# Kernel optimization log

Measured on AMD Instinct MI355X. Metric: run time of the kernel, lower is better.

The kernel has to match this reference:

```python
import jax, jax.numpy as jnp
import numpy as np
import math

EPS = 1e-7
K_NEIGHBORS = 32  # matches init kwarg k

def _project(x, c):
    norm = jnp.linalg.norm(x, axis=-1, keepdims=True).clip(EPS)
    sqrt_c = jnp.sqrt(c).clip(EPS)
    max_norm = (1.0 - EPS) / sqrt_c
    return x * jnp.minimum(max_norm / norm, 1.0)

def _mobius_add(x, y, c):
    x2 = jnp.sum(x * x, axis=-1, keepdims=True)
    y2 = jnp.sum(y * y, axis=-1, keepdims=True)
    xy = jnp.sum(x * y, axis=-1, keepdims=True)
    num = (1 + 2 * c * xy + c * y2) * x + (1 - c * x2) * y
    den = 1 + 2 * c * xy + c * c * x2 * y2
    return _project(num / den.clip(EPS), c)

def _dist(x, y, c):
    sqrt_c = jnp.sqrt(c).clip(EPS)
    diff = _mobius_add(x, -y, c)
    dn = jnp.linalg.norm(diff, axis=-1)
    arg = jnp.minimum(sqrt_c * dn.clip(EPS, 1 - EPS), 1.0 - EPS)
    return 2.0 * jnp.arctanh(arg) / sqrt_c

def _logmap0(y, c):
    sqrt_c = jnp.sqrt(c).clip(EPS)
    yn = jnp.linalg.norm(y, axis=-1, keepdims=True)
    is_zero = yn < EPS
    syn = yn.clip(EPS)
    arg = jnp.minimum(sqrt_c * syn, 1.0 - EPS)
    mag = jnp.arctanh(arg) / sqrt_c
    return jnp.where(is_zero, jnp.zeros_like(y), mag * y / syn)

def _layernorm(x, g, b):
    m = x.mean(-1, keepdims=True)
    v = x.var(-1, keepdims=True)
    return (x - m) / jnp.sqrt(v + 1e-6) * g + b

def setup_inputs() -> dict:
    key = jax.random.key(0)
    B, N, D, P, H = 2, 2048, 512, 3, 8
    ks = jax.random.split(key, 16)
    s = 0.02
    d = {}
    d['x'] = jax.random.normal(ks[0], (B, N, D), dtype=jnp.float32)
    d['positions'] = jax.random.normal(ks[1], (B, N, P), dtype=jnp.float32) * 0.1
    d['c'] = jnp.float32(1.0)
    d['Wq'] = jax.random.normal(ks[2], (D, D), jnp.float32) * s; d['bq'] = jnp.zeros((D,), jnp.float32)
    d['Wk'] = jax.random.normal(ks[3], (D, D), jnp.float32) * s; d['bk'] = jnp.zeros((D,), jnp.float32)
    d['Wv'] = jax.random.normal(ks[4], (D, D), jnp.float32) * s; d['bv'] = jnp.zeros((D,), jnp.float32)
    d['Wg'] = jax.random.normal(ks[5], (P, D), jnp.float32) * s; d['bg'] = jnp.zeros((D,), jnp.float32)
    d['Wo'] = jax.random.normal(ks[6], (D, D), jnp.float32) * s; d['bo'] = jnp.zeros((D,), jnp.float32)
    d['Wf1'] = jax.random.normal(ks[7], (D, 4 * D), jnp.float32) * s; d['bf1'] = jnp.zeros((4 * D,), jnp.float32)
    d['Wf2'] = jax.random.normal(ks[8], (4 * D, D), jnp.float32) * s; d['bf2'] = jnp.zeros((D,), jnp.float32)
    d['g1'] = jnp.ones((D,), jnp.float32); d['b1'] = jnp.zeros((D,), jnp.float32)
    d['g2'] = jnp.ones((D,), jnp.float32); d['b2'] = jnp.zeros((D,), jnp.float32)
    d['ascale'] = jnp.ones((H,), jnp.float32)
    d['fscale'] = jnp.ones((H,), jnp.float32)
    return d

def reference(x, positions, c, Wq, bq, Wk, bk, Wv, bv, Wg, bg, Wo, bo, Wf1, bf1, Wf2, bf2, g1, b1, g2, b2, ascale, fscale):
    B, N, D = x.shape
    H = ascale.shape[0]
    hd = D // H
    K = K_NEIGHBORS

    xn = _layernorm(x, g1, b1)
    q = (xn @ Wq + bq).reshape(B, N, H, hd)
    k = (xn @ Wk + bk).reshape(B, N, H, hd)
    v = (xn @ Wv + bv).reshape(B, N, H, hd)

    # full pairwise hyperbolic distance matrix [B, N, N]
    dmat = _dist(positions[:, :, None, :], positions[:, None, :, :], c)
    idx = jax.lax.top_k(-dmat, K)[1]  # [B, N, K]

    bidx = jnp.arange(B)[:, None, None]
    key_pos = positions[bidx, idx]                 # [B, N, K, P]
    qpos = positions[:, :, None, :]                # [B, N, 1, P]
    geo = _logmap0(_mobius_add(-qpos, key_pos, c), c)
    geo_v = (geo @ Wg + bg).reshape(B, N, K, H, hd)

    kg = k[bidx, idx]                              # [B, N, K, H, hd]
    vg = v[bidx, idx]

    align = jnp.einsum('bnhd,bnkhd->bhnk', q, geo_v)
    feat = jnp.einsum('bnhd,bnkhd->bhnk', q, kg) / math.sqrt(hd)
    scores = fscale[None, :, None, None] * feat + ascale[None, :, None, None] * align
    w = jax.nn.softmax(scores.astype(jnp.float32), axis=-1)
    attn = jnp.einsum('bhnk,bnkhd->bnhd', w, vg).reshape(B, N, D)

    x1 = x + attn @ Wo + bo
    h = _layernorm(x1, g2, b2)
    x2 = x1 + jax.nn.gelu(h @ Wf1 + bf1) @ Wf2 + bf2
    return x2
```

## Files before the change

kernel.cpp:

```cpp
#include <hip/hip_runtime.h>
#include <math.h>

#define EPSF 1e-7f

constexpr int Bb = 2, Nn = 2048, Dd = 512, Hh = 8, HD = 64, KK = 32;
constexpr int ROWS = Bb * Nn;

typedef __attribute__((ext_vector_type(8))) short bf16x8;
typedef __attribute__((ext_vector_type(4))) float f32x4;
typedef __attribute__((ext_vector_type(8))) unsigned short u16x8;
typedef unsigned long long u64;

__device__ inline unsigned short f2bf(float f) {
    union { float f; unsigned int u; } v; v.f = f;
    unsigned int u = v.u;
    unsigned int r = (u + 0x7fffu + ((u >> 16) & 1u)) >> 16;
    return (unsigned short)r;
}

__device__ inline float bf2f(short s) {
    union { unsigned int u; float f; } x;
    x.u = ((unsigned int)(unsigned short)s) << 16;
    return x.f;
}

__device__ inline float gelu_tanh(float v) {
    float u = v + 0.044715f * v * v * v;
    return 0.5f * v * (1.f + tanhf(0.79788456080286535588f * u));
}

__device__ __forceinline__ void tcvt(float (*tile)[65], const float* __restrict__ in,
                                     unsigned short* __restrict__ out,
                                     int K, int N, int bx, int by) {
    int k0 = by * 64, n0 = bx * 64;
    int t = threadIdx.x;
    int lr = t >> 6, lc = t & 63;
#pragma unroll 4
    for (int p = 0; p < 16; ++p) {
        int r = p * 4 + lr;
        tile[r][lc] = in[(size_t)(k0 + r) * N + n0 + lc];
    }
    __syncthreads();
#pragma unroll 4
    for (int p = 0; p < 16; ++p) {
        int n = p * 4 + lr;
        out[(size_t)(n0 + n) * K + k0 + lc] = f2bf(tile[lc][n]);
    }
}

__device__ __forceinline__ void ln_row(const float* __restrict__ x,
                                       const float* __restrict__ g,
                                       const float* __restrict__ b,
                                       unsigned short* __restrict__ out,
                                       int row, int lane) {
    const float* xr = x + (size_t)row * Dd;
    float4 v0 = *(const float4*)(xr + lane * 8);
    float4 v1 = *(const float4*)(xr + lane * 8 + 4);
    float s = v0.x + v0.y + v0.z + v0.w + v1.x + v1.y + v1.z + v1.w;
    float s2 = v0.x * v0.x + v0.y * v0.y + v0.z * v0.z + v0.w * v0.w +
               v1.x * v1.x + v1.y * v1.y + v1.z * v1.z + v1.w * v1.w;
    for (int o = 32; o; o >>= 1) { s += __shfl_xor(s, o); s2 += __shfl_xor(s2, o); }
    float mean = s * (1.f / Dd);
    float var = s2 * (1.f / Dd) - mean * mean;
    float rstd = rsqrtf(var + 1e-6f);
    float4 g0 = *(const float4*)(g + lane * 8);
    float4 g1v = *(const float4*)(g + lane * 8 + 4);
    float4 b0 = *(const float4*)(b + lane * 8);
    float4 b1v = *(const float4*)(b + lane * 8 + 4);
    u16x8 o;
    o[0] = f2bf((v0.x - mean) * rstd * g0.x + b0.x);
    o[1] = f2bf((v0.y - mean) * rstd * g0.y + b0.y);
    o[2] = f2bf((v0.z - mean) * rstd * g0.z + b0.z);
    o[3] = f2bf((v0.w - mean) * rstd * g0.w + b0.w);
    o[4] = f2bf((v1.x - mean) * rstd * g1v.x + b1v.x);
    o[5] = f2bf((v1.y - mean) * rstd * g1v.y + b1v.y);
    o[6] = f2bf((v1.z - mean) * rstd * g1v.z + b1v.z);
    o[7] = f2bf((v1.w - mean) * rstd * g1v.w + b1v.w);
    *(u16x8*)(out + (size_t)row * Dd + lane * 8) = o;
}

__global__ __launch_bounds__(256) void ln_kernel(const float* __restrict__ x,
                                                 const float* __restrict__ g,
                                                 const float* __restrict__ b,
                                                 unsigned short* __restrict__ out) {
    ln_row(x, g, b, out, blockIdx.x * 4 + (threadIdx.x >> 6), threadIdx.x & 63);
}

__global__ __launch_bounds__(256) void prep_kernel(
    const float* __restrict__ Wq, const float* __restrict__ Wk,
    const float* __restrict__ Wv, const float* __restrict__ Wo,
    const float* __restrict__ Wf1, const float* __restrict__ Wf2,
    const float* __restrict__ bq, const float* __restrict__ bk, const float* __restrict__ bv,
    const float* __restrict__ x, const float* __restrict__ g1, const float* __restrict__ b1,
    unsigned short* __restrict__ wqkv_t, unsigned short* __restrict__ wo_t,
    unsigned short* __restrict__ wf1_t, unsigned short* __restrict__ wf2_t,
    float* __restrict__ bqkv, unsigned short* __restrict__ xn) {
    __shared__ float tile[64][65];
    int bid = blockIdx.x;
    if (bid < 256) {
        int z = bid >> 6, r = bid & 63;
        const float* in = (z == 0) ? Wq : (z == 1) ? Wk : (z == 2) ? Wv : Wo;
        unsigned short* out = (z == 0) ? wqkv_t : (z == 1) ? wqkv_t + 262144
                            : (z == 2) ? wqkv_t + 524288 : wo_t;
        tcvt(tile, in, out, 512, 512, r & 7, r >> 3);
    } else if (bid < 512) {
        int r = bid - 256;
        tcvt(tile, Wf1, wf1_t, 512, 2048, r & 31, r >> 5);
    } else if (bid < 768) {
        int r = bid - 512;
        tcvt(tile, Wf2, wf2_t, 2048, 512, r & 7, r >> 3);
    } else if (bid < 774) {
        int t = (bid - 768) * 256 + threadIdx.x;
        if (t < 512) bqkv[t] = bq[t];
        else if (t < 1024) bqkv[t] = bk[t - 512];
        else if (t < 1536) bqkv[t] = bv[t - 1024];
    } else {
        ln_row(x, g1, b1, xn, (bid - 774) * 4 + (threadIdx.x >> 6), threadIdx.x & 63);
    }
}

template <int EPI, int OBF16>
__device__ __forceinline__ void gemm64_body(short* __restrict__ As, short* __restrict__ Bs,
                                            const unsigned short* __restrict__ A,
                                            const unsigned short* __restrict__ Bt,
                                            const float* __restrict__ bias,
                                            const float* __restrict__ resid,
                                            void* __restrict__ C,
                                            int N, int K, int gridX, int nwg, int wgid) {
    int cpx = nwg >> 3;
    int nid = (wgid & 7) * cpx + (wgid >> 3);
    int bx = nid % gridX, by = nid / gridX;
    int bm = by * 64, bn = bx * 64;
    int tid = threadIdx.x;
    int wave = tid >> 6, lane = tid & 63;
    int wr = wave >> 1, wc = wave & 1;
    f32x4 acc[2][2] = {};

    int srow = wave * 8 + (lane >> 3);
    int scol = ((lane & 7) ^ (lane >> 3)) * 8;
    const unsigned short* gA0 = A + (size_t)(bm + srow) * K + scol;
    const unsigned short* gA1 = A + (size_t)(bm + srow + 32) * K + scol;
    const unsigned short* gB0 = Bt + (size_t)(bn + srow) * K + scol;
    const unsigned short* gB1 = Bt + (size_t)(bn + srow + 32) * K + scol;

#define STAGE(buf, kof)                                                                                 \
    do {                                                                                                \
        __builtin_amdgcn_global_load_lds((const __attribute__((address_space(1))) void*)(gA0 + (kof)), \
            (__attribute__((address_space(3))) void*)(As + (buf) * 4096 + wave * 512), 16, 0, 0);       \
        __builtin_amdgcn_global_load_lds((const __attribute__((address_space(1))) void*)(gA1 + (kof)), \
            (__attribute__((address_space(3))) void*)(As + (buf) * 4096 + 2048 + wave * 512), 16, 0, 0);\
        __builtin_amdgcn_global_load_lds((const __attribute__((address_space(1))) void*)(gB0 + (kof)), \
            (__attribute__((address_space(3))) void*)(Bs + (buf) * 4096 + wave * 512), 16, 0, 0);       \
        __builtin_amdgcn_global_load_lds((const __attribute__((address_space(1))) void*)(gB1 + (kof)), \
            (__attribute__((address_space(3))) void*)(Bs + (buf) * 4096 + 2048 + wave * 512), 16, 0, 0);\
    } while (0)

    int nt = K >> 6;
    int cur = 0;
    STAGE(0, 0);
    __syncthreads();
    for (int t = 0; t < nt; ++t) {
        if (t + 1 < nt) STAGE(cur ^ 1, (t + 1) * 64);
        const short* as = As + cur * 4096;
        const short* bs = Bs + cur * 4096;
#pragma unroll
        for (int kk = 0; kk < 64; kk += 32) {
            int kx = (kk + (lane >> 4) * 8) ^ ((lane & 7) << 3);
            bf16x8 a0 = *(const bf16x8*)(as + (wr * 32 + (lane & 15)) * 64 + kx);
            bf16x8 a1 = *(const bf16x8*)(as + (wr * 32 + 16 + (lane & 15)) * 64 + kx);
            bf16x8 b0 = *(const bf16x8*)(bs + (wc * 32 + (lane & 15)) * 64 + kx);
            bf16x8 b1 = *(const bf16x8*)(bs + (wc * 32 + 16 + (lane & 15)) * 64 + kx);
            acc[0][0] = __builtin_amdgcn_mfma_f32_16x16x32_bf16(a0, b0, acc[0][0], 0, 0, 0);
            acc[0][1] = __builtin_amdgcn_mfma_f32_16x16x32_bf16(a0, b1, acc[0][1], 0, 0, 0);
            acc[1][0] = __builtin_amdgcn_mfma_f32_16x16x32_bf16(a1, b0, acc[1][0], 0, 0, 0);
            acc[1][1] = __builtin_amdgcn_mfma_f32_16x16x32_bf16(a1, b1, acc[1][1], 0, 0, 0);
        }
        __syncthreads();
        cur ^= 1;
    }
#undef STAGE

    int cbase = bn + wc * 32 + (lane & 15);
    int rbase = bm + wr * 32 + (lane >> 4) * 4;
    float bias_v[2] = {bias[cbase], bias[cbase + 16]};
#pragma unroll
    for (int mi = 0; mi < 2; ++mi) {
#pragma unroll
        for (int r = 0; r < 4; ++r) {
            int row = rbase + mi * 16 + r;
#pragma unroll
            for (int ni = 0; ni < 2; ++ni) {
                int col = cbase + ni * 16;
                float v = acc[mi][ni][r] + bias_v[ni];
                if (EPI == 1) v += resid[(size_t)row * N + col];
                if (EPI == 2) v = gelu_tanh(v);
                if (OBF16) ((unsigned short*)C)[(size_t)row * N + col] = f2bf(v);
                else ((float*)C)[(size_t)row * N + col] = v;
            }
        }
    }
}

template <int EPI, int OBF16>
__global__ __launch_bounds__(256) void gemm64(const unsigned short* __restrict__ A,
                                              const unsigned short* __restrict__ Bt,
                                              const float* __restrict__ bias,
                                              const float* __restrict__ resid,
                                              void* __restrict__ C,
                                              int N, int K, int gridX) {
    __shared__ short As[2 * 64 * 64];
    __shared__ short Bs[2 * 64 * 64];
    gemm64_body<EPI, OBF16>(As, Bs, A, Bt, bias, resid, C, N, K, gridX, gridDim.x, blockIdx.x);
}

template <int CTRL>
__device__ inline u64 dpp_u64(u64 v) {
    int lo = (int)(unsigned int)v;
    int hi = (int)(unsigned int)(v >> 32);
    lo = __builtin_amdgcn_update_dpp(lo, lo, CTRL, 0xF, 0xF, false);
    hi = __builtin_amdgcn_update_dpp(hi, hi, CTRL, 0xF, 0xF, false);
    return ((u64)(unsigned int)hi << 32) | (unsigned int)lo;
}

__device__ inline u64 wave_min_u64(u64 v) {
    u64 o;
    o = dpp_u64<0xB1>(v);  if (o < v) v = o;
    o = dpp_u64<0x4E>(v);  if (o < v) v = o;
    o = dpp_u64<0x141>(v); if (o < v) v = o;
    o = dpp_u64<0x140>(v); if (o < v) v = o;
    o = __shfl_xor(v, 16); if (o < v) v = o;
    o = __shfl_xor(v, 32); if (o < v) v = o;
    return v;
}

__device__ __forceinline__ void topk_body(char* smem, const float* __restrict__ pos,
                                          const float* __restrict__ cp,
                                          int* __restrict__ idx_out, int bid) {
    float* s_px = (float*)smem;
    float* s_py = s_px + Nn;
    float* s_pz = s_py + Nn;
    float* s_u  = s_pz + Nn;
    int* s_out  = (int*)(s_u + Nn);
    int b = bid >> 9;
    int q0 = (bid & 511) * 4;
    int t = threadIdx.x;
    float c = *cp;
    const float* pb = pos + (size_t)b * Nn * 3;
    for (int j = t; j < Nn; j += 256) {
        float px = pb[j * 3 + 0], py = pb[j * 3 + 1], pz = pb[j * 3 + 2];
        s_px[j] = px; s_py[j] = py; s_pz[j] = pz;
        s_u[j] = c * (px * px + py * py + pz * pz);
    }
    __syncthreads();
    int wave = t >> 6, lane = t & 63;
    int n = q0 + wave;
    float qx = s_px[n], qy = s_py[n], qz = s_pz[n];
    float cx2 = s_u[n];
    float x2 = cx2 / c;
    float B = 1.f - cx2;
    float rc = 1.f / c;
    float B2rc = B * B * rc;
    float m2c = -2.f * c;
    float m2B = -2.f * B;
    float key[32];
#pragma unroll
    for (int i = 0; i < 32; ++i) {
        int j = i * 64 + lane;
        float dot = qx * s_px[j] + qy * s_py[j] + qz * s_pz[j];
        float su = s_u[j];
        float r = fmaf(m2c, dot, 1.f);
        float A = r + su;
        float den = fmaf(cx2, su, r);
        float p1 = x2 * A;
        float q1 = A * dot;
        float t1 = fmaf(m2B, q1, B2rc * su);
        float num2 = fmaf(p1, A, t1);
        float rd = __builtin_amdgcn_rcpf(den);
        key[i] = num2 * rd * rd;
    }
    const u64 MAXK = ~0ull;
    u64 B0 = MAXK, B1 = MAXK, B2 = MAXK, B3 = MAXK;
#pragma unroll
    for (int i = 0; i < 32; ++i) {
        u64 k = ((u64)__float_as_uint(key[i]) << 32) | (unsigned int)(i * 64 + lane);
        if (k < B3) {
            B3 = k;
            if (B3 < B2) { u64 tmp = B2; B2 = B3; B3 = tmp; }
            if (B2 < B1) { u64 tmp = B1; B1 = B2; B2 = tmp; }
            if (B1 < B0) { u64 tmp = B0; B0 = B1; B1 = tmp; }
        }
    }
    int bcount = 4, consumed = 0;
    u64 last = 0;
    for (int s2 = 0; s2 < KK; ++s2) {
        bool need = (bcount == 0) && (consumed < 32);
        if (__any(need)) {
            if (need) {
                B0 = MAXK; B1 = MAXK; B2 = MAXK; B3 = MAXK;
#pragma unroll
                for (int i = 0; i < 32; ++i) {
                    u64 k = ((u64)__float_as_uint(key[i]) << 32) | (unsigned int)(i * 64 + lane);
                    if (k > last && k < B3) {
                        B3 = k;
                        if (B3 < B2) { u64 tmp = B2; B2 = B3; B3 = tmp; }
                        if (B2 < B1) { u64 tmp = B1; B1 = B2; B2 = tmp; }
                        if (B1 < B0) { u64 tmp = B0; B0 = B1; B1 = tmp; }
                    }
                }
                int rem = 32 - consumed;
                bcount = rem < 4 ? rem : 4;
            }
        }
        u64 offer = (bcount > 0) ? B0 : MAXK;
        u64 g = wave_min_u64(offer);
        if (lane == 0) s_out[wave * KK + s2] = (int)(unsigned int)g;
        if (offer == g) {
            B0 = B1; B1 = B2; B2 = B3; B3 = MAXK;
            --bcount; ++consumed; last = g;
        }
    }
    if (lane < KK) idx_out[(size_t)(b * Nn + n) * KK + lane] = s_out[wave * KK + lane];
}

__global__ __launch_bounds__(256) void qkv_topk_kernel(const unsigned short* __restrict__ A,
                                                       const unsigned short* __restrict__ Wqkv,
                                                       const float* __restrict__ bqkv,
                                                       unsigned short* __restrict__ qkv,
                                                       const float* __restrict__ pos,
                                                       const float* __restrict__ cp,
                                                       int* __restrict__ idx_out) {
    __shared__ __align__(16) char smem[33280];
    if (blockIdx.x < 1536) {
        short* As = (short*)smem;
        short* Bs = (short*)(smem + 16384);
        gemm64_body<0, 1>(As, Bs, A, Wqkv, bqkv, nullptr, qkv, 1536, 512, 24, 1536, blockIdx.x);
    } else {
        topk_body(smem, pos, cp, idx_out, blockIdx.x - 1536);
    }
}

__global__ __launch_bounds__(256) void attn_kernel(const unsigned short* __restrict__ qkv,
                                                   const int* __restrict__ idx,
                                                   const float* __restrict__ pos,
                                                   const float* __restrict__ Wg,
                                                   const float* __restrict__ bg,
                                                   const float* __restrict__ ascale,
                                                   const float* __restrict__ fscale,
                                                   const float* __restrict__ cp,
                                                   unsigned short* __restrict__ out) {
    constexpr int QS = 1536;
    int bid = blockIdx.x;
    int xcd = bid & 7, slot = bid >> 3;
    int b = xcd >> 2;
    int n = (xcd & 3) * 512 + slot;
    int bn = b * Nn + n;
    int t = threadIdx.x;
    int wave = t >> 6, lane = t & 63;
    __shared__ float s_q[Dd];
    __shared__ float s_geo[KK][3];
    __shared__ int s_idx[KK];
    __shared__ float s_qg[Hh][3];
    __shared__ float s_qb[Hh];
    __shared__ float s_dot[KK][9];
    __shared__ float s_w[Hh][KK];
    __shared__ float s_part[4][Dd];
    float c = *cp;
    if (t >= 64 && t < 96) s_idx[t - 64] = idx[(size_t)bn * KK + (t - 64)];
    if (t < 64) {
        bf16x8 q8 = *(const bf16x8*)(qkv + (size_t)bn * QS + t * 8);
#pragma unroll
        for (int j = 0; j < 8; ++j) s_q[t * 8 + j] = bf2f(q8[j]);
    }
    __syncthreads();
    if (t < KK) {
        const float* qp = pos + (size_t)bn * 3;
        const float* kp = pos + (size_t)(b * Nn + s_idx[t]) * 3;
        float xx = -qp[0], xyc = -qp[1], xz = -qp[2];
        float yx = kp[0], yy = kp[1], yz = kp[2];
        float x2 = xx * xx + xyc * xyc + xz * xz;
        float y2 = yx * yx + yy * yy + yz * yz;
        float xy = xx * yx + xyc * yy + xz * yz;
        float Av = 1.f + 2.f * c * xy + c * y2;
        float Bv = 1.f - c * x2;
        float den = fmaxf(1.f + 2.f * c * xy + c * c * x2 * y2, EPSF);
        float mx = (Av * xx + Bv * yx) / den;
        float my = (Av * xyc + Bv * yy) / den;
        float mz = (Av * xz + Bv * yz) / den;
        float rn = fmaxf(sqrtf(mx * mx + my * my + mz * mz), EPSF);
        float sqrt_c = fmaxf(sqrtf(c), EPSF);
        float max_norm = (1.f - EPSF) / sqrt_c;
        float scpr = fminf(max_norm / rn, 1.f);
        mx *= scpr; my *= scpr; mz *= scpr;
        float yn = sqrtf(mx * mx + my * my + mz * mz);
        if (yn < EPSF) {
            s_geo[t][0] = 0.f; s_geo[t][1] = 0.f; s_geo[t][2] = 0.f;
        } else {
            float syn = fmaxf(yn, EPSF);
            float arg = fminf(sqrt_c * syn, 1.f - EPSF);
            float mag = atanhf(arg) / sqrt_c;
            float f = mag / syn;
            s_geo[t][0] = mx * f; s_geo[t][1] = my * f; s_geo[t][2] = mz * f;
        }
    } else if (t >= 64 && t < 88) {
        int h = (t - 64) / 3, p = (t - 64) % 3;
        float acc = 0.f;
        for (int d2 = 0; d2 < HD; ++d2) acc += s_q[h * HD + d2] * Wg[p * Dd + h * HD + d2];
        s_qg[h][p] = acc;
    } else if (t >= 96 && t < 104) {
        int h = t - 96;
        float acc = 0.f;
        for (int d2 = 0; d2 < HD; ++d2) acc += s_q[h * HD + d2] * bg[h * HD + d2];
        s_qb[h] = acc;
    }
    {
#pragma unroll
        for (int r = 0; r < 8; ++r) {
            int kk = wave * 8 + r;
            int nk = s_idx[kk];
            bf16x8 k8 = *(const bf16x8*)(qkv + (size_t)(b * Nn + nk) * QS + 512 + lane * 8);
            float p = 0.f;
#pragma unroll
            for (int j = 0; j < 8; ++j) p = fmaf(bf2f(k8[j]), s_q[lane * 8 + j], p);
            p += __shfl_xor(p, 1);
            p += __shfl_xor(p, 2);
            p += __shfl_xor(p, 4);
            if ((lane & 7) == 0) s_dot[kk][lane >> 3] = p;
        }
    }
    __syncthreads();
    {
        int h = t >> 5, kk = t & 31;
        float align = s_geo[kk][0] * s_qg[h][0] + s_geo[kk][1] * s_qg[h][1] +
                      s_geo[kk][2] * s_qg[h][2] + s_qb[h];
        float scv = fscale[h] * s_dot[kk][h] * 0.125f + ascale[h] * align;
        float m = scv;
        for (int o = 16; o; o >>= 1) m = fmaxf(m, __shfl_xor(m, o));
        float e = expf(scv - m);
        float ss = e;
        for (int o = 16; o; o >>= 1) ss += __shfl_xor(ss, o);
        s_w[h][kk] = e / ss;
    }
    __syncthreads();
    {
        float acc[8] = {0.f, 0.f, 0.f, 0.f, 0.f, 0.f, 0.f, 0.f};
        int h = lane >> 3;
#pragma unroll
        for (int r = 0; r < 8; ++r) {
            int kk = wave * 8 + r;
            int nk = s_idx[kk];
            bf16x8 v8 = *(const bf16x8*)(qkv + (size_t)(b * Nn + nk) * QS + 1024 + lane * 8);
            float wgt = s_w[h][kk];
#pragma unroll
            for (int j = 0; j < 8; ++j) acc[j] = fmaf(bf2f(v8[j]), wgt, acc[j]);
        }
#pragma unroll
        for (int j = 0; j < 8; ++j) s_part[wave][lane * 8 + j] = acc[j];
    }
    __syncthreads();
    for (int d = t; d < Dd; d += 256) {
        float s = s_part[0][d] + s_part[1][d] + s_part[2][d] + s_part[3][d];
        out[(size_t)bn * Dd + d] = f2bf(s);
    }
}

extern "C" void kernel_launch(void* const* d_in, const int* in_sizes, int n_in,
                              void* d_out, int out_size, void* d_ws, size_t ws_size,
                              hipStream_t stream) {
    const float* x   = (const float*)d_in[0];
    const float* pos = (const float*)d_in[1];
    const float* cp  = (const float*)d_in[2];
    const float* Wq  = (const float*)d_in[3];
    const float* bq  = (const float*)d_in[4];
    const float* Wk  = (const float*)d_in[5];
    const float* bk  = (const float*)d_in[6];
    const float* Wv  = (const float*)d_in[7];
    const float* bv  = (const float*)d_in[8];
    const float* Wg  = (const float*)d_in[9];
    const float* bg  = (const float*)d_in[10];
    const float* Wo  = (const float*)d_in[11];
    const float* bo  = (const float*)d_in[12];
    const float* Wf1 = (const float*)d_in[13];
    const float* bf1 = (const float*)d_in[14];
    const float* Wf2 = (const float*)d_in[15];
    const float* bf2 = (const float*)d_in[16];
    const float* g1  = (const float*)d_in[17];
    const float* b1  = (const float*)d_in[18];
    const float* g2  = (const float*)d_in[19];
    const float* b2  = (const float*)d_in[20];
    const float* asc = (const float*)d_in[21];
    const float* fsc = (const float*)d_in[22];
    float* out = (float*)d_out;
    char* ws = (char*)d_ws;

    unsigned short* qkv_bf  = (unsigned short*)(ws + 0);
    unsigned short* t_bf    = (unsigned short*)(ws + 0);
    unsigned short* xn_bf   = (unsigned short*)(ws + 25165824);
    float*          x1      = (float*)(ws + 29360128);
    unsigned short* attn_bf = (unsigned short*)(ws + 37748736);
    unsigned short* wqkv_t  = (unsigned short*)(ws + 41943040);
    unsigned short* wo_t    = (unsigned short*)(ws + 43515904);
    unsigned short* wf1_t   = (unsigned short*)(ws + 44040192);
    unsigned short* wf2_t   = (unsigned short*)(ws + 46137344);
    int*            idx     = (int*)(ws + 48234496);
    float*          bqkv    = (float*)(ws + 48758784);

    prep_kernel<<<1798, 256, 0, stream>>>(Wq, Wk, Wv, Wo, Wf1, Wf2, bq, bk, bv,
                                          x, g1, b1, wqkv_t, wo_t, wf1_t, wf2_t, bqkv, xn_bf);
    qkv_topk_kernel<<<2560, 256, 0, stream>>>(xn_bf, wqkv_t, bqkv, qkv_bf, pos, cp, idx);
    attn_kernel<<<ROWS, 256, 0, stream>>>(qkv_bf, idx, pos, Wg, bg, asc, fsc, cp, attn_bf);
    gemm64<1, 0><<<512, 256, 0, stream>>>(attn_bf, wo_t, bo, x, x1, 512, 512, 8);
    ln_kernel<<<ROWS / 4, 256, 0, stream>>>(x1, g2, b2, xn_bf);
    gemm64<2, 1><<<2048, 256, 0, stream>>>(xn_bf, wf1_t, bf1, nullptr, t_bf, 2048, 512, 32);
    gemm64<1, 0><<<512, 256, 0, stream>>>(t_bf, wf2_t, bf2, x1, out, 512, 2048, 8);
}
```

Baseline: 138.3 us.

## Split fused QKV/topk kernel, use 32-bit wave min, prefetch V rows

Result: no change. 138.9 us (+0.5%).

```diff
diff --git a/kernel.cpp b/kernel.cpp
--- a/kernel.cpp
+++ b/kernel.cpp
@@ -120,14 +120,17 @@
 }
 
 template <int EPI, int OBF16>
-__device__ __forceinline__ void gemm64_body(short* __restrict__ As, short* __restrict__ Bs,
-                                            const unsigned short* __restrict__ A,
-                                            const unsigned short* __restrict__ Bt,
-                                            const float* __restrict__ bias,
-                                            const float* __restrict__ resid,
-                                            void* __restrict__ C,
-                                            int N, int K, int gridX, int nwg, int wgid) {
+__global__ __launch_bounds__(256) void gemm64(const unsigned short* __restrict__ A,
+                                              const unsigned short* __restrict__ Bt,
+                                              const float* __restrict__ bias,
+                                              const float* __restrict__ resid,
+                                              void* __restrict__ C,
+                                              int N, int K, int gridX) {
+    __shared__ short As[2 * 64 * 64];
+    __shared__ short Bs[2 * 64 * 64];
+    int nwg = gridDim.x;
     int cpx = nwg >> 3;
+    int wgid = blockIdx.x;
     int nid = (wgid & 7) * cpx + (wgid >> 3);
     int bx = nid % gridX, by = nid / gridX;
     int bm = by * 64, bn = bx * 64;
@@ -201,48 +204,44 @@
     }
 }
 
-template <int EPI, int OBF16>
-__global__ __launch_bounds__(256) void gemm64(const unsigned short* __restrict__ A,
-                                              const unsigned short* __restrict__ Bt,
-                                              const float* __restrict__ bias,
-                                              const float* __restrict__ resid,
-                                              void* __restrict__ C,
-                                              int N, int K, int gridX) {
-    __shared__ short As[2 * 64 * 64];
-    __shared__ short Bs[2 * 64 * 64];
-    gemm64_body<EPI, OBF16>(As, Bs, A, Bt, bias, resid, C, N, K, gridX, gridDim.x, blockIdx.x);
-}
-
 template <int CTRL>
-__device__ inline u64 dpp_u64(u64 v) {
-    int lo = (int)(unsigned int)v;
-    int hi = (int)(unsigned int)(v >> 32);
-    lo = __builtin_amdgcn_update_dpp(lo, lo, CTRL, 0xF, 0xF, false);
-    hi = __builtin_amdgcn_update_dpp(hi, hi, CTRL, 0xF, 0xF, false);
-    return ((u64)(unsigned int)hi << 32) | (unsigned int)lo;
-}
-
-__device__ inline u64 wave_min_u64(u64 v) {
-    u64 o;
-    o = dpp_u64<0xB1>(v);  if (o < v) v = o;
-    o = dpp_u64<0x4E>(v);  if (o < v) v = o;
-    o = dpp_u64<0x141>(v); if (o < v) v = o;
-    o = dpp_u64<0x140>(v); if (o < v) v = o;
-    o = __shfl_xor(v, 16); if (o < v) v = o;
-    o = __shfl_xor(v, 32); if (o < v) v = o;
+__device__ inline float dpp_f(float v) {
+    int i = __float_as_int(v);
+    i = __builtin_amdgcn_update_dpp(i, i, CTRL, 0xF, 0xF, false);
+    return __int_as_float(i);
+}
+template <int CTRL>
+__device__ inline unsigned dpp_u(unsigned v) {
+    return (unsigned)__builtin_amdgcn_update_dpp((int)v, (int)v, CTRL, 0xF, 0xF, false);
+}
+
+__device__ inline float wave_min_f32(float v) {
+    v = fminf(v, dpp_f<0xB1>(v));
+    v = fminf(v, dpp_f<0x4E>(v));
+    v = fminf(v, dpp_f<0x141>(v));
+    v = fminf(v, dpp_f<0x140>(v));
+    v = fminf(v, __shfl_xor(v, 16));
+    v = fminf(v, __shfl_xor(v, 32));
     return v;
 }
-
-__device__ __forceinline__ void topk_body(char* smem, const float* __restrict__ pos,
-                                          const float* __restrict__ cp,
-                                          int* __restrict__ idx_out, int bid) {
-    float* s_px = (float*)smem;
-    float* s_py = s_px + Nn;
-    float* s_pz = s_py + Nn;
-    float* s_u  = s_pz + Nn;
-    int* s_out  = (int*)(s_u + Nn);
-    int b = bid >> 9;
-    int q0 = (bid & 511) * 4;
+__device__ inline unsigned wave_min_u32(unsigned v) {
+    unsigned o;
+    o = dpp_u<0xB1>(v);  v = o < v ? o : v;
+    o = dpp_u<0x4E>(v);  v = o < v ? o : v;
+    o = dpp_u<0x141>(v); v = o < v ? o : v;
+    o = dpp_u<0x140>(v); v = o < v ? o : v;
+    o = __shfl_xor(v, 16); v = o < v ? o : v;
+    o = __shfl_xor(v, 32); v = o < v ? o : v;
+    return v;
+}
+
+__global__ __launch_bounds__(256, 4) void topk_kernel(const float* __restrict__ pos,
+                                                      const float* __restrict__ cp,
+                                                      int* __restrict__ idx_out) {
+    __shared__ float s_px[Nn], s_py[Nn], s_pz[Nn], s_u[Nn];
+    __shared__ int s_out[4][KK];
+    int b = blockIdx.x >> 9;
+    int q0 = (blockIdx.x & 511) * 4;
     int t = threadIdx.x;
     float c = *cp;
     const float* pb = pos + (size_t)b * Nn * 3;
@@ -276,7 +275,7 @@
         float t1 = fmaf(m2B, q1, B2rc * su);
         float num2 = fmaf(p1, A, t1);
         float rd = __builtin_amdgcn_rcpf(den);
-        key[i] = num2 * rd * rd;
+        key[i] = fmaf(num2, rd * rd, 1.0f);
     }
     const u64 MAXK = ~0ull;
     u64 B0 = MAXK, B1 = MAXK, B2 = MAXK, B3 = MAXK;
@@ -312,31 +311,25 @@
             }
         }
         u64 offer = (bcount > 0) ? B0 : MAXK;
-        u64 g = wave_min_u64(offer);
-        if (lane == 0) s_out[wave * KK + s2] = (int)(unsigned int)g;
-        if (offer == g) {
+        float okey = __uint_as_float((unsigned)(offer >> 32));
+        unsigned oidx = (unsigned)offer;
+        float m = wave_min_f32(okey);
+        u64 mask = __ballot(okey == m);
+        unsigned gidx;
+        if (__popcll(mask) == 1) {
+            gidx = (unsigned)__shfl((int)oidx, __ffsll(mask) - 1);
+        } else {
+            unsigned cand = ((mask >> lane) & 1ull) ? oidx : 0xFFFFFFFFu;
+            gidx = wave_min_u32(cand);
+        }
+        if (lane == 0) s_out[wave][s2] = (int)gidx;
+        if (okey == m && oidx == gidx) {
             B0 = B1; B1 = B2; B2 = B3; B3 = MAXK;
-            --bcount; ++consumed; last = g;
-        }
-    }
-    if (lane < KK) idx_out[(size_t)(b * Nn + n) * KK + lane] = s_out[wave * KK + lane];
-}
-
-__global__ __launch_bounds__(256) void qkv_topk_kernel(const unsigned short* __restrict__ A,
-                                                       const unsigned short* __restrict__ Wqkv,
-                                                       const float* __restrict__ bqkv,
-                                                       unsigned short* __restrict__ qkv,
-                                                       const float* __restrict__ pos,
-                                                       const float* __restrict__ cp,
-                                                       int* __restrict__ idx_out) {
-    __shared__ __align__(16) char smem[33280];
-    if (blockIdx.x < 1536) {
-        short* As = (short*)smem;
-        short* Bs = (short*)(smem + 16384);
-        gemm64_body<0, 1>(As, Bs, A, Wqkv, bqkv, nullptr, qkv, 1536, 512, 24, 1536, blockIdx.x);
-    } else {
-        topk_body(smem, pos, cp, idx_out, blockIdx.x - 1536);
-    }
+            --bcount; ++consumed;
+            last = ((u64)__float_as_uint(m) << 32) | gidx;
+        }
+    }
+    if (lane < KK) idx_out[(size_t)(b * Nn + n) * KK + lane] = s_out[wave][lane];
 }
 
 __global__ __launch_bounds__(256) void attn_kernel(const unsigned short* __restrict__ qkv,
@@ -412,6 +405,7 @@
         for (int d2 = 0; d2 < HD; ++d2) acc += s_q[h * HD + d2] * bg[h * HD + d2];
         s_qb[h] = acc;
     }
+    bf16x8 v8r[8];
     {
 #pragma unroll
         for (int r = 0; r < 8; ++r) {
@@ -425,6 +419,11 @@
             p += __shfl_xor(p, 2);
             p += __shfl_xor(p, 4);
             if ((lane & 7) == 0) s_dot[kk][lane >> 3] = p;
+        }
+#pragma unroll
+        for (int r = 0; r < 8; ++r) {
+            int nk = s_idx[wave * 8 + r];
+            v8r[r] = *(const bf16x8*)(qkv + (size_t)(b * Nn + nk) * QS + 1024 + lane * 8);
         }
     }
     __syncthreads();
@@ -446,12 +445,9 @@
         int h = lane >> 3;
 #pragma unroll
         for (int r = 0; r < 8; ++r) {
-            int kk = wave * 8 + r;
-            int nk = s_idx[kk];
-            bf16x8 v8 = *(const bf16x8*)(qkv + (size_t)(b * Nn + nk) * QS + 1024 + lane * 8);
-            float wgt = s_w[h][kk];
-#pragma unroll
-            for (int j = 0; j < 8; ++j) acc[j] = fmaf(bf2f(v8[j]), wgt, acc[j]);
+            float wgt = s_w[h][wave * 8 + r];
+#pragma unroll
+            for (int j = 0; j < 8; ++j) acc[j] = fmaf(bf2f(v8r[r][j]), wgt, acc[j]);
         }
 #pragma unroll
         for (int j = 0; j < 8; ++j) s_part[wave][lane * 8 + j] = acc[j];
@@ -506,7 +502,8 @@
 
     prep_kernel<<<1798, 256, 0, stream>>>(Wq, Wk, Wv, Wo, Wf1, Wf2, bq, bk, bv,
                                           x, g1, b1, wqkv_t, wo_t, wf1_t, wf2_t, bqkv, xn_bf);
-    qkv_topk_kernel<<<2560, 256, 0, stream>>>(xn_bf, wqkv_t, bqkv, qkv_bf, pos, cp, idx);
+    topk_kernel<<<ROWS / 4, 256, 0, stream>>>(pos, cp, idx);
+    gemm64<0, 1><<<1536, 256, 0, stream>>>(xn_bf, wqkv_t, bqkv, nullptr, qkv_bf, 1536, 512, 24);
     attn_kernel<<<ROWS, 256, 0, stream>>>(qkv_bf, idx, pos, Wg, bg, asc, fsc, cp, attn_bf);
     gemm64<1, 0><<<512, 256, 0, stream>>>(attn_bf, wo_t, bo, x, x1, 512, 512, 8);
     ln_kernel<<<ROWS / 4, 256, 0, stream>>>(x1, g2, b2, xn_bf);
```
